# Optimization experiments

Measured on AMD Instinct MI355X. Metric: run time of the kernel, lower is better.

## Reference

```python
import jax, jax.numpy as jnp
import numpy as np

N_NODES = 500_000
N_EDGES = 5_000_000


def _glorot(key, shape):
    fan_in, fan_out = shape[0], shape[1]
    s = jnp.sqrt(6.0 / (fan_in + fan_out))
    return jax.random.uniform(key, shape, jnp.float32, -s, s)


def setup_inputs() -> dict:
    key = jax.random.key(0)
    ks = jax.random.split(key, 16)
    x = jax.random.normal(ks[0], (N_NODES, 3), jnp.float32)
    edge_index = jax.random.randint(ks[1], (2, N_EDGES), 0, N_NODES, jnp.int64)
    dims = [(3, 16), (16, 16), (16, 1)]
    inp = {"x": x, "edge_index": edge_index}
    for i, (din, dout) in enumerate(dims, start=1):
        k = jax.random.split(ks[1 + i], 5)
        inp[f"p{i}_w"] = _glorot(k[0], (din, din))   # project lin (bias=True)
        inp[f"p{i}_b"] = jnp.zeros((din,), jnp.float32)
        inp[f"l{i}_w"] = _glorot(k[1], (din, dout))  # lin_l on aggregated neighbors (bias=True)
        inp[f"l{i}_b"] = jnp.zeros((dout,), jnp.float32)
        inp[f"r{i}_w"] = _glorot(k[2], (din, dout))  # lin_r on root (bias=False)
    return inp


def _sage_conv(x, src, dst, pw, pb, lw, lb, rw):
    # project=True: neighbor messages use relu(lin(x)); root term uses original x
    h = jax.nn.relu(x @ pw + pb)                    # [N, din]
    msg = jnp.take(h, src, axis=0)                  # [E, din] gather from source j
    agg = jax.ops.segment_sum(msg, dst, num_segments=N_NODES)  # scatter-add to target i
    return agg @ lw + lb + x @ rw                   # [N, dout]


def reference(x, edge_index, p1_w, p1_b, l1_w, l1_b, r1_w,
              p2_w, p2_b, l2_w, l2_b, r2_w,
              p3_w, p3_b, l3_w, l3_b, r3_w):
    src, dst = edge_index[0], edge_index[1]
    h = jax.nn.relu(_sage_conv(x, src, dst, p1_w, p1_b, l1_w, l1_b, r1_w))
    h = jax.nn.relu(_sage_conv(h, src, dst, p2_w, p2_b, l2_w, l2_b, r2_w))
    return jax.nn.sigmoid(_sage_conv(h, src, dst, p3_w, p3_b, l3_w, l3_b, r3_w))
```

## Files before the change

### kernel.cpp

```cpp
#include <hip/hip_runtime.h>
#include <hip/hip_fp16.h>
#include <math.h>

#define NN 500000
#define NE 5000000
#define K_B 977
#define NBP 500
#define EPB 10000
#define CAP 6144
#define SEG 3072
#define PH 16
#define PHW 32768

__device__ inline float2 cvt2(unsigned u) {
    __half2 h = *reinterpret_cast<const __half2*>(&u);
    return __half22float2(h);
}

__device__ inline int wave_iscan(int x, int lane) {
#pragma unroll
    for (int d = 1; d < 64; d <<= 1) {
        int u = __shfl_up(x, d);
        if (lane >= d) x += u;
    }
    return x;
}


__global__ __launch_bounds__(512) void part_kernel(
    const int* __restrict__ ei, int* __restrict__ counts,
    unsigned int* __restrict__ edg_staged,
    const float* __restrict__ x, const float* __restrict__ p1w,
    const float* __restrict__ p1b, __half* __restrict__ h1)
{
    __shared__ unsigned stage[EPB];
    __shared__ int hist[1024];
    __shared__ int wsum[8];
    int t = threadIdx.x, j = blockIdx.x;
    int e0 = j * EPB;
    hist[t] = 0; hist[t + 512] = 0;
    __syncthreads();
    for (int k = t; k < EPB; k += 512) {
        int d = ei[NE + e0 + k];
        atomicAdd(&hist[d >> 9], 1);
    }
    __syncthreads();
    int v0 = hist[2*t], v1 = hist[2*t+1];
    int sv2 = v0 + v1;
    int lane = t & 63, w = t >> 6;
    int inc = wave_iscan(sv2, lane);
    if (lane == 63) wsum[w] = inc;
    __syncthreads();
    if (t == 0) {
        int run = 0;
#pragma unroll
        for (int i = 0; i < 8; ++i) { int tm = wsum[i]; wsum[i] = run; run += tm; }
    }
    __syncthreads();
    int excl = inc - sv2 + wsum[w];
    hist[2*t] = excl;
    hist[2*t+1] = excl + v0;
    if (2*t < K_B)   counts[j*K_B + 2*t]   = excl;
    if (2*t+1 < K_B) counts[j*K_B + 2*t+1] = excl + v0;
    __syncthreads();
    for (int k = t; k < EPB; k += 512) {
        int e = e0 + k;
        int sv = ei[e];
        int d = ei[NE + e];
        int pos = atomicAdd(&hist[d >> 9], 1);
        stage[pos] = ((unsigned)(d & 511) << 20) | (unsigned)sv;
    }
    __syncthreads();
    for (int k = t; k < EPB; k += 512)
        edg_staged[e0 + k] = stage[k];
    for (int i = j * 1000 + t; i < j * 1000 + 1000; i += 512) {
        float x0 = x[i*3+0], x1 = x[i*3+1], x2v = x[i*3+2];
        __half hh[4];
#pragma unroll
        for (int jj = 0; jj < 3; ++jj) {
            float v = fmaf(x0, p1w[0*3+jj], fmaf(x1, p1w[1*3+jj], fmaf(x2v, p1w[2*3+jj], p1b[jj])));
            hh[jj] = __float2half(v > 0.f ? v : 0.f);
        }
        hh[3] = __float2half(0.f);
        *reinterpret_cast<uint2*>(h1 + (size_t)i * 4) = *reinterpret_cast<uint2*>(hh);
    }
}


__global__ __launch_bounds__(512) void csrfin_l1(
    const int* __restrict__ counts,
    const unsigned int* __restrict__ edg_staged,
    const __half* __restrict__ h1, const float* __restrict__ x,
    const float* __restrict__ l1w, const float* __restrict__ l1b,
    const float* __restrict__ r1w,
    const float* __restrict__ p2w, const float* __restrict__ p2b,
    unsigned int* __restrict__ edg_fin, unsigned int* __restrict__ rowptr,
    __half* __restrict__ X2, __half* __restrict__ H2)
{
    __shared__ unsigned ebuf[CAP];
    __shared__ unsigned ebuf2[CAP];
    __shared__ unsigned cnt[4096];
    __shared__ int wsum[8];
    __shared__ int sh_total;
    __shared__ float slw[48], srw[48], slb[16], sp2w[256], sp2b[16];
    int b = blockIdx.x, t = threadIdx.x;
    if (t < 256) sp2w[t] = p2w[t];
    if (t < 48) { slw[t] = l1w[t]; srw[t] = r1w[t]; }
    if (t < 16) { slb[t] = l1b[t]; sp2b[t] = p2b[t]; }
    int pj = 0, lj = 0;
    if (t < NBP) {
        int base = t * K_B;
        int w0 = counts[base + b];
        int nx = (b == K_B - 1) ? EPB : counts[base + b + 1];
        pj = t * EPB + w0;
        lj = nx - w0;
    }
    int lane = t & 63, w = t >> 6;
    int inc = wave_iscan(lj, lane);
    if (lane == 63) wsum[w] = inc;
    __syncthreads();
    if (t == 0) {
        int run = 0;
#pragma unroll
        for (int i = 0; i < 8; ++i) { int tm = wsum[i]; wsum[i] = run; run += tm; }
        sh_total = run;
    }
    cnt[t] = 0; cnt[t + 512] = 0; cnt[t + 1024] = 0; cnt[t + 1536] = 0;
    cnt[t + 2048] = 0; cnt[t + 2560] = 0; cnt[t + 3072] = 0; cnt[t + 3584] = 0;
    __syncthreads();
    int poff = inc - lj + wsum[w];
    {
        int k = 0;
        for (; k + 4 <= lj; k += 4) {
            unsigned a0 = edg_staged[pj + k + 0];
            unsigned a1 = edg_staged[pj + k + 1];
            unsigned a2 = edg_staged[pj + k + 2];
            unsigned a3 = edg_staged[pj + k + 3];
            int p = poff + k;
            if (p + 3 < CAP) {
                ebuf[p + 0] = a0; ebuf[p + 1] = a1;
                ebuf[p + 2] = a2; ebuf[p + 3] = a3;
            } else {
                if (p + 0 < CAP) ebuf[p + 0] = a0;
                if (p + 1 < CAP) ebuf[p + 1] = a1;
                if (p + 2 < CAP) ebuf[p + 2] = a2;
                if (p + 3 < CAP) ebuf[p + 3] = a3;
            }
        }
        for (; k < lj; ++k) {
            int p = poff + k;
            if (p < CAP) ebuf[p] = edg_staged[pj + k];
        }
    }
    __syncthreads();
    int n2 = sh_total; if (n2 > CAP) n2 = CAP;
    for (int k = t; k < n2; k += 512) {
        unsigned v = ebuf[k];
        unsigned bin = ((v >> 20) << 4) | ((v & 0xFFFFFu) >> 15);
        atomicAdd(&cnt[bin >> 1], (bin & 1u) ? 65536u : 1u);
    }
    __syncthreads();
    unsigned wlo[8];
#pragma unroll
    for (int q = 0; q < 8; ++q) wlo[q] = cnt[t * 8 + q];
    int myc = 0;
#pragma unroll
    for (int q = 0; q < 8; ++q) myc += (int)(wlo[q] & 0xFFFFu) + (int)(wlo[q] >> 16);
    int inc2 = wave_iscan(myc, lane);
    if (lane == 63) wsum[w] = inc2;
    __syncthreads();
    if (t == 0) {
        int run = 0;
#pragma unroll
        for (int i = 0; i < 8; ++i) { int tm = wsum[i]; wsum[i] = run; run += tm; }
    }
    __syncthreads();
    int excl = inc2 - myc + wsum[w];
    int node = (b << 9) + t;
    unsigned gbase = (unsigned)(b * CAP + excl);
    if (node < NN) rowptr[node] = (gbase << 9) | (unsigned)myc;
    {
        int run2 = excl;
#pragma unroll
        for (int q = 0; q < 8; ++q) {
            int c0 = (int)(wlo[q] & 0xFFFFu), c1 = (int)(wlo[q] >> 16);
            cnt[t * 8 + q] = (unsigned)run2 | ((unsigned)(run2 + c0) << 16);
            run2 += c0 + c1;
        }
    }
    __syncthreads();
    for (int k = t; k < n2; k += 512) {
        unsigned v = ebuf[k];
        unsigned src = v & 0xFFFFFu;
        unsigned bin = ((v >> 20) << 4) | (src >> 15);
        unsigned old = atomicAdd(&cnt[bin >> 1], (bin & 1u) ? 65536u : 1u);
        unsigned pos = (bin & 1u) ? (old >> 16) : (old & 0xFFFFu);
        ebuf2[pos] = src;
    }
    __syncthreads();
    int bbase = b * CAP;
    for (int k = t; k < n2; k += 512) edg_fin[bbase + k] = ebuf2[k];
    if (node >= NN) return;
    float a0 = 0.f, a1 = 0.f, a2 = 0.f;
    for (int k = 0; k < myc; ++k) {
        unsigned s = ebuf2[excl + k];
        uint2 r = *reinterpret_cast<const uint2*>(h1 + (size_t)s * 4);
        float2 p0 = cvt2(r.x), q0 = cvt2(r.y);
        a0 += p0.x; a1 += p0.y; a2 += q0.x;
    }
    float x0 = x[node*3+0], x1 = x[node*3+1], x2v = x[node*3+2];
    float h[16];
#pragma unroll
    for (int j = 0; j < 16; ++j) {
        float v = slb[j];
        v = fmaf(a0, slw[j], fmaf(a1, slw[16+j], fmaf(a2, slw[32+j], v)));
        v = fmaf(x0, srw[j], fmaf(x1, srw[16+j], fmaf(x2v, srw[32+j], v)));
        h[j] = v > 0.f ? v : 0.f;
    }
    __half hx[16];
#pragma unroll
    for (int j = 0; j < 16; ++j) hx[j] = __float2half(h[j]);
    uint4* xp = reinterpret_cast<uint4*>(X2 + (size_t)node * 16);
    xp[0] = reinterpret_cast<uint4*>(hx)[0];
    xp[1] = reinterpret_cast<uint4*>(hx)[1];
    __half hh[16];
#pragma unroll
    for (int j = 0; j < 16; ++j) {
        float v = sp2b[j];
#pragma unroll
        for (int k = 0; k < 16; ++k) v = fmaf(h[k], sp2w[k*16+j], v);
        hh[j] = __float2half(v > 0.f ? v : 0.f);
    }
    uint4* hp = reinterpret_cast<uint4*>(H2 + (size_t)node * 16);
    hp[0] = reinterpret_cast<uint4*>(hh)[0];
    hp[1] = reinterpret_cast<uint4*>(hh)[1];
}


__global__ __launch_bounds__(256, 8) void layer2_kernel(
    const unsigned int* __restrict__ rowptr, const unsigned int* __restrict__ edg,
    const __half* __restrict__ H2, __half* X ,
    const float* __restrict__ l2w, const float* __restrict__ l2b,
    const float* __restrict__ r2w,
    const float* __restrict__ p3w, const float* __restrict__ p3b,
    const float* __restrict__ l3w, __half* __restrict__ g)
{
    __shared__ float slw[256], srw[256], sp3w[256];
    __shared__ float slb[16], sp3b[16], sl3w[16];
    __shared__ unsigned sedg[SEG];
    __shared__ int sred[256];
    int t = threadIdx.x;
    slw[t] = l2w[t]; srw[t] = r2w[t]; sp3w[t] = p3w[t];
    if (t < 16) { slb[t] = l2b[t]; sp3b[t] = p3b[t]; sl3w[t] = l3w[t]; }
    int i = blockIdx.x * 256 + t;
    bool act = i < NN;
    unsigned rp = act ? rowptr[i] : 0;
    int beg = (int)(rp >> 9), deg = act ? (int)(rp & 511u) : 0;
    sred[t] = act ? (beg + deg) : 0;
    __syncthreads();
    int base = (int)(rowptr[blockIdx.x * 256] >> 9);
    for (int off = 128; off > 0; off >>= 1) {
        if (t < off) { int o = sred[t + off]; if (o > sred[t]) sred[t] = o; }
        __syncthreads();
    }
    int seglen = sred[0] - base;
    if (seglen > SEG) seglen = SEG;
    for (int k = t; k < seglen; k += 256) sedg[k] = edg[base + k];
    __syncthreads();
    int e = beg - base, eend = e + deg;
    if (eend > SEG) eend = SEG;
    float av[16];
#pragma unroll
    for (int k = 0; k < 16; ++k) av[k] = 0.f;
#pragma unroll 1
    for (int p = 1; p <= PH; ++p) {
        unsigned lim = (unsigned)(p * PHW);
        while (e < eend) {
            unsigned s0 = sedg[e];
            if (s0 >= lim) break;
            const uint4* r0 = reinterpret_cast<const uint4*>(H2 + (size_t)s0 * 16);
            uint4 A0 = r0[0], B0 = r0[1];
            float2 f;
            f = cvt2(A0.x); av[0] += f.x; av[1] += f.y;
            f = cvt2(A0.y); av[2] += f.x; av[3] += f.y;
            f = cvt2(A0.z); av[4] += f.x; av[5] += f.y;
            f = cvt2(A0.w); av[6] += f.x; av[7] += f.y;
            f = cvt2(B0.x); av[8] += f.x; av[9] += f.y;
            f = cvt2(B0.y); av[10] += f.x; av[11] += f.y;
            f = cvt2(B0.z); av[12] += f.x; av[13] += f.y;
            f = cvt2(B0.w); av[14] += f.x; av[15] += f.y;
            ++e;
        }
        __syncthreads();
    }
    if (!act) return;
    float xv[16];
    const uint4* xp = reinterpret_cast<const uint4*>(X + (size_t)i * 16);
    uint4 XA = xp[0], XB = xp[1];
    {
        float2 f;
        f = cvt2(XA.x); xv[0] = f.x; xv[1] = f.y;
        f = cvt2(XA.y); xv[2] = f.x; xv[3] = f.y;
        f = cvt2(XA.z); xv[4] = f.x; xv[5] = f.y;
        f = cvt2(XA.w); xv[6] = f.x; xv[7] = f.y;
        f = cvt2(XB.x); xv[8] = f.x; xv[9] = f.y;
        f = cvt2(XB.y); xv[10] = f.x; xv[11] = f.y;
        f = cvt2(XB.z); xv[12] = f.x; xv[13] = f.y;
        f = cvt2(XB.w); xv[14] = f.x; xv[15] = f.y;
    }
    float o[16];
#pragma unroll
    for (int j = 0; j < 16; ++j) {
        float v = slb[j];
#pragma unroll
        for (int k = 0; k < 16; ++k) v = fmaf(av[k], slw[k*16+j], v);
#pragma unroll
        for (int k = 0; k < 16; ++k) v = fmaf(xv[k], srw[k*16+j], v);
        o[j] = v > 0.f ? v : 0.f;
    }
    __half ho[16];
#pragma unroll
    for (int j = 0; j < 16; ++j) ho[j] = __float2half(o[j]);
    uint4* op = reinterpret_cast<uint4*>(X + (size_t)i * 16);
    op[0] = reinterpret_cast<uint4*>(ho)[0];
    op[1] = reinterpret_cast<uint4*>(ho)[1];
    float gg = 0.f;
#pragma unroll
    for (int j = 0; j < 16; ++j) {
        float u = sp3b[j];
#pragma unroll
        for (int k = 0; k < 16; ++k) u = fmaf(o[k], sp3w[k*16+j], u);
        u = u > 0.f ? u : 0.f;
        gg = fmaf(u, sl3w[j], gg);
    }
    g[i] = __float2half(gg);
}


__global__ __launch_bounds__(256) void layer3_kernel(
    const unsigned int* __restrict__ rowptr, const unsigned int* __restrict__ edg,
    const __half* __restrict__ g, const __half* __restrict__ X,
    const float* __restrict__ l3b, const float* __restrict__ r3w,
    float* __restrict__ out)
{
    __shared__ float srw[16];
    __shared__ float sb;
    int t = threadIdx.x;
    if (t < 16) srw[t] = r3w[t];
    if (t == 0) sb = l3b[0];
    __syncthreads();
    int i = blockIdx.x * 256 + t;
    if (i >= NN) return;
    unsigned rp = rowptr[i];
    int beg = (int)(rp >> 9), deg = (int)(rp & 511u);
    int end = beg + deg;
    float a = 0.f;
    int e = beg;
    for (; e + 1 < end; e += 2) {
        int s0 = (int)edg[e], s1 = (int)edg[e+1];
        __half g0 = g[s0], g1 = g[s1];
        a += __half2float(g0) + __half2float(g1);
    }
    if (e < end) a += __half2float(g[(int)edg[e]]);
    float val = a + sb;
    const uint4* xp = reinterpret_cast<const uint4*>(X + (size_t)i * 16);
    uint4 XA = xp[0], XB = xp[1];
    float2 f;
    f = cvt2(XA.x); val = fmaf(f.x, srw[0], fmaf(f.y, srw[1], val));
    f = cvt2(XA.y); val = fmaf(f.x, srw[2], fmaf(f.y, srw[3], val));
    f = cvt2(XA.z); val = fmaf(f.x, srw[4], fmaf(f.y, srw[5], val));
    f = cvt2(XA.w); val = fmaf(f.x, srw[6], fmaf(f.y, srw[7], val));
    f = cvt2(XB.x); val = fmaf(f.x, srw[8], fmaf(f.y, srw[9], val));
    f = cvt2(XB.y); val = fmaf(f.x, srw[10], fmaf(f.y, srw[11], val));
    f = cvt2(XB.z); val = fmaf(f.x, srw[12], fmaf(f.y, srw[13], val));
    f = cvt2(XB.w); val = fmaf(f.x, srw[14], fmaf(f.y, srw[15], val));
    out[i] = 1.f / (1.f + expf(-val));
}


extern "C" void kernel_launch(void* const* d_in, const int* in_sizes, int n_in,
                              void* d_out, int out_size, void* d_ws, size_t ws_size,
                              hipStream_t stream) {
    const float* x   = (const float*)d_in[0];
    const int*   ei  = (const int*)d_in[1];
    const float* p1w = (const float*)d_in[2];
    const float* p1b = (const float*)d_in[3];
    const float* l1w = (const float*)d_in[4];
    const float* l1b = (const float*)d_in[5];
    const float* r1w = (const float*)d_in[6];
    const float* p2w = (const float*)d_in[7];
    const float* p2b = (const float*)d_in[8];
    const float* l2w = (const float*)d_in[9];
    const float* l2b = (const float*)d_in[10];
    const float* r2w = (const float*)d_in[11];
    const float* p3w = (const float*)d_in[12];
    const float* p3b = (const float*)d_in[13];
    const float* l3w = (const float*)d_in[14];
    const float* l3b = (const float*)d_in[15];
    const float* r3w = (const float*)d_in[16];
    float* out = (float*)d_out;

    char* ws = (char*)d_ws;
    __half*       X        = (__half*)(ws);
    __half*       H2       = (__half*)(ws + 16000000);
    unsigned int* edg_stg  = (unsigned int*)(ws + 32000000);
    unsigned int* edg_fin  = (unsigned int*)(ws + 52000000);
    __half*       h1       = (__half*)(ws + 76012288);
    __half*       g        = (__half*)(ws + 80012288);
    unsigned int* rowptr   = (unsigned int*)(ws + 81012288);
    int*          counts   = (int*)(ws + 83012288);

    const int nbN = (NN + 255) / 256;

    part_kernel<<<NBP, 512, 0, stream>>>(ei, counts, edg_stg, x, p1w, p1b, h1);
    csrfin_l1<<<K_B, 512, 0, stream>>>(counts, edg_stg, h1, x,
                                       l1w, l1b, r1w, p2w, p2b,
                                       edg_fin, rowptr, X, H2);
    layer2_kernel<<<nbN, 256, 0, stream>>>(rowptr, edg_fin, H2, X,
                                           l2w, l2b, r2w, p3w, p3b, l3w, g);
    layer3_kernel<<<nbN, 256, 0, stream>>>(rowptr, edg_fin, g, X, l3b, r3w, out);
}
```

Before: 178.8 us.

## Aggregate layer-1 neighbor features edge-parallel with LDS atomics

Layer-1 aggregation used to loop serially per destination node over its edges, which leaves threads idle when degrees are uneven. It now runs edge-parallel across the block: each thread handles two edges per step, gathers the fp16 source features, and adds them into a shared-memory per-destination accumulator with atomics. The sorted edge buffer now keeps the full packed value so the destination is available, and a barrier is added before nodes read their sums. This trades serial per-node loops for LDS float atomic contention and one extra sync, and the summation order is no longer deterministic.

```diff
diff --git a/kernel.cpp b/kernel.cpp
--- a/kernel.cpp
+++ b/kernel.cpp
@@ -100,6 +100,7 @@
     __shared__ unsigned ebuf[CAP];
     __shared__ unsigned ebuf2[CAP];
     __shared__ unsigned cnt[4096];
+    __shared__ float acc[3 * 512];
     __shared__ int wsum[8];
     __shared__ int sh_total;
     __shared__ float slw[48], srw[48], slb[16], sp2w[256], sp2b[16];
@@ -107,6 +108,7 @@
     if (t < 256) sp2w[t] = p2w[t];
     if (t < 48) { slw[t] = l1w[t]; srw[t] = r1w[t]; }
     if (t < 16) { slb[t] = l1b[t]; sp2b[t] = p2b[t]; }
+    acc[t] = 0.f; acc[t + 512] = 0.f; acc[t + 1024] = 0.f;
     int pj = 0, lj = 0;
     if (t < NBP) {
         int base = t * K_B;
@@ -191,23 +193,47 @@
     __syncthreads();
     for (int k = t; k < n2; k += 512) {
         unsigned v = ebuf[k];
-        unsigned src = v & 0xFFFFFu;
-        unsigned bin = ((v >> 20) << 4) | (src >> 15);
+        unsigned bin = ((v >> 20) << 4) | ((v & 0xFFFFFu) >> 15);
         unsigned old = atomicAdd(&cnt[bin >> 1], (bin & 1u) ? 65536u : 1u);
         unsigned pos = (bin & 1u) ? (old >> 16) : (old & 0xFFFFu);
-        ebuf2[pos] = src;
+        ebuf2[pos] = v;
     }
     __syncthreads();
     int bbase = b * CAP;
-    for (int k = t; k < n2; k += 512) edg_fin[bbase + k] = ebuf2[k];
+    {
+        int k = t;
+        for (; k + 512 < n2; k += 1024) {
+            unsigned v0 = ebuf2[k], v1 = ebuf2[k + 512];
+            unsigned s0 = v0 & 0xFFFFFu, s1 = v1 & 0xFFFFFu;
+            edg_fin[bbase + k] = s0;
+            edg_fin[bbase + k + 512] = s1;
+            int d0 = (int)(v0 >> 20), d1 = (int)(v1 >> 20);
+            uint2 r0 = *reinterpret_cast<const uint2*>(h1 + (size_t)s0 * 4);
+            uint2 r1 = *reinterpret_cast<const uint2*>(h1 + (size_t)s1 * 4);
+            float2 p0 = cvt2(r0.x), q0 = cvt2(r0.y);
+            atomicAdd(&acc[d0], p0.x);
+            atomicAdd(&acc[512 + d0], p0.y);
+            atomicAdd(&acc[1024 + d0], q0.x);
+            float2 p1 = cvt2(r1.x), q1 = cvt2(r1.y);
+            atomicAdd(&acc[d1], p1.x);
+            atomicAdd(&acc[512 + d1], p1.y);
+            atomicAdd(&acc[1024 + d1], q1.x);
+        }
+        if (k < n2) {
+            unsigned v0 = ebuf2[k];
+            unsigned s0 = v0 & 0xFFFFFu;
+            edg_fin[bbase + k] = s0;
+            int d0 = (int)(v0 >> 20);
+            uint2 r0 = *reinterpret_cast<const uint2*>(h1 + (size_t)s0 * 4);
+            float2 p0 = cvt2(r0.x), q0 = cvt2(r0.y);
+            atomicAdd(&acc[d0], p0.x);
+            atomicAdd(&acc[512 + d0], p0.y);
+            atomicAdd(&acc[1024 + d0], q0.x);
+        }
+    }
+    __syncthreads();
     if (node >= NN) return;
-    float a0 = 0.f, a1 = 0.f, a2 = 0.f;
-    for (int k = 0; k < myc; ++k) {
-        unsigned s = ebuf2[excl + k];
-        uint2 r = *reinterpret_cast<const uint2*>(h1 + (size_t)s * 4);
-        float2 p0 = cvt2(r.x), q0 = cvt2(r.y);
-        a0 += p0.x; a1 += p0.y; a2 += q0.x;
-    }
+    float a0 = acc[t], a1 = acc[512 + t], a2 = acc[1024 + t];
     float x0 = x[node*3+0], x1 = x[node*3+1], x2v = x[node*3+2];
     float h[16];
 #pragma unroll
```

After: 255.4 us. 42.8% more time.

## Process two rows per thread in layer2 and align blocks to CSR partitions

Applied to the files above, without the earlier changes.

The layer-2 kernel now has each 256-thread block cover 512 nodes, one CSR partition of CAP edges. Each thread aggregates two rows with interleaved gather loops. The block loads its edge segment straight from the known partition base, which drops the max-reduction over row ends and the SEG truncation. The source-index phase loop goes from 16 phases of 32768 to 8 phases of 65536, so there are fewer barriers. Occupancy is lowered to 5 blocks per CU and register pressure rises from the doubled accumulators, in exchange for more memory-level parallelism per thread.

```diff
diff --git a/kernel.cpp b/kernel.cpp
--- a/kernel.cpp
+++ b/kernel.cpp
@@ -8,9 +8,7 @@
 #define NBP 500
 #define EPB 10000
 #define CAP 6144
-#define SEG 3072
-#define PH 16
-#define PHW 32768
+#define PH 8
 
 __device__ inline float2 cvt2(unsigned u) {
     __half2 h = *reinterpret_cast<const __half2*>(&u);
@@ -237,63 +235,12 @@
 }
 
 
-__global__ __launch_bounds__(256, 8) void layer2_kernel(
-    const unsigned int* __restrict__ rowptr, const unsigned int* __restrict__ edg,
-    const __half* __restrict__ H2, __half* X ,
-    const float* __restrict__ l2w, const float* __restrict__ l2b,
-    const float* __restrict__ r2w,
-    const float* __restrict__ p3w, const float* __restrict__ p3b,
-    const float* __restrict__ l3w, __half* __restrict__ g)
+__device__ inline void l2_row(int i, const float* av,
+                              const float* slw, const float* srw,
+                              const float* slb, const float* sp3w,
+                              const float* sp3b, const float* sl3w,
+                              __half* X, __half* g)
 {
-    __shared__ float slw[256], srw[256], sp3w[256];
-    __shared__ float slb[16], sp3b[16], sl3w[16];
-    __shared__ unsigned sedg[SEG];
-    __shared__ int sred[256];
-    int t = threadIdx.x;
-    slw[t] = l2w[t]; srw[t] = r2w[t]; sp3w[t] = p3w[t];
-    if (t < 16) { slb[t] = l2b[t]; sp3b[t] = p3b[t]; sl3w[t] = l3w[t]; }
-    int i = blockIdx.x * 256 + t;
-    bool act = i < NN;
-    unsigned rp = act ? rowptr[i] : 0;
-    int beg = (int)(rp >> 9), deg = act ? (int)(rp & 511u) : 0;
-    sred[t] = act ? (beg + deg) : 0;
-    __syncthreads();
-    int base = (int)(rowptr[blockIdx.x * 256] >> 9);
-    for (int off = 128; off > 0; off >>= 1) {
-        if (t < off) { int o = sred[t + off]; if (o > sred[t]) sred[t] = o; }
-        __syncthreads();
-    }
-    int seglen = sred[0] - base;
-    if (seglen > SEG) seglen = SEG;
-    for (int k = t; k < seglen; k += 256) sedg[k] = edg[base + k];
-    __syncthreads();
-    int e = beg - base, eend = e + deg;
-    if (eend > SEG) eend = SEG;
-    float av[16];
-#pragma unroll
-    for (int k = 0; k < 16; ++k) av[k] = 0.f;
-#pragma unroll 1
-    for (int p = 1; p <= PH; ++p) {
-        unsigned lim = (unsigned)(p * PHW);
-        while (e < eend) {
-            unsigned s0 = sedg[e];
-            if (s0 >= lim) break;
-            const uint4* r0 = reinterpret_cast<const uint4*>(H2 + (size_t)s0 * 16);
-            uint4 A0 = r0[0], B0 = r0[1];
-            float2 f;
-            f = cvt2(A0.x); av[0] += f.x; av[1] += f.y;
-            f = cvt2(A0.y); av[2] += f.x; av[3] += f.y;
-            f = cvt2(A0.z); av[4] += f.x; av[5] += f.y;
-            f = cvt2(A0.w); av[6] += f.x; av[7] += f.y;
-            f = cvt2(B0.x); av[8] += f.x; av[9] += f.y;
-            f = cvt2(B0.y); av[10] += f.x; av[11] += f.y;
-            f = cvt2(B0.z); av[12] += f.x; av[13] += f.y;
-            f = cvt2(B0.w); av[14] += f.x; av[15] += f.y;
-            ++e;
-        }
-        __syncthreads();
-    }
-    if (!act) return;
     float xv[16];
     const uint4* xp = reinterpret_cast<const uint4*>(X + (size_t)i * 16);
     uint4 XA = xp[0], XB = xp[1];
@@ -334,6 +281,78 @@
         gg = fmaf(u, sl3w[j], gg);
     }
     g[i] = __float2half(gg);
+}
+
+__global__ __launch_bounds__(256, 5) void layer2_kernel(
+    const unsigned int* __restrict__ rowptr, const unsigned int* __restrict__ edg,
+    const __half* __restrict__ H2, __half* X ,
+    const float* __restrict__ l2w, const float* __restrict__ l2b,
+    const float* __restrict__ r2w,
+    const float* __restrict__ p3w, const float* __restrict__ p3b,
+    const float* __restrict__ l3w, __half* __restrict__ g)
+{
+    __shared__ float slw[256], srw[256], sp3w[256];
+    __shared__ float slb[16], sp3b[16], sl3w[16];
+    __shared__ unsigned sedg[CAP];
+    int t = threadIdx.x, b = blockIdx.x;
+    slw[t] = l2w[t]; srw[t] = r2w[t]; sp3w[t] = p3w[t];
+    if (t < 16) { slb[t] = l2b[t]; sp3b[t] = p3b[t]; sl3w[t] = l3w[t]; }
+    int base = b * CAP;
+    int iA = b * 512 + t;
+    int iB = iA + 256;
+    bool actB = iB < NN;
+    unsigned rpA = rowptr[iA];
+    unsigned rpB = actB ? rowptr[iB] : 0;
+    int eA = (int)(rpA >> 9) - base, dgA = (int)(rpA & 511u);
+    int eB = actB ? ((int)(rpB >> 9) - base) : 0, dgB = actB ? (int)(rpB & 511u) : 0;
+    int endA = eA + dgA, endB = eB + dgB;
+    int lastn = (b * 512 + 511 < NN) ? (b * 512 + 511) : (NN - 1);
+    unsigned rpl = rowptr[lastn];
+    int n2 = (int)(rpl >> 9) + (int)(rpl & 511u) - base;
+    for (int k = t; k < n2; k += 256) sedg[k] = edg[base + k];
+    __syncthreads();
+    float avA[16], avB[16];
+#pragma unroll
+    for (int k = 0; k < 16; ++k) { avA[k] = 0.f; avB[k] = 0.f; }
+#pragma unroll 1
+    for (int p = 1; p <= PH; ++p) {
+        unsigned lim = (unsigned)(p << 16);
+        while (eA < endA) {
+            unsigned s0 = sedg[eA];
+            if (s0 >= lim) break;
+            const uint4* r0 = reinterpret_cast<const uint4*>(H2 + (size_t)s0 * 16);
+            uint4 A0 = r0[0], B0 = r0[1];
+            float2 f;
+            f = cvt2(A0.x); avA[0] += f.x; avA[1] += f.y;
+            f = cvt2(A0.y); avA[2] += f.x; avA[3] += f.y;
+            f = cvt2(A0.z); avA[4] += f.x; avA[5] += f.y;
+            f = cvt2(A0.w); avA[6] += f.x; avA[7] += f.y;
+            f = cvt2(B0.x); avA[8] += f.x; avA[9] += f.y;
+            f = cvt2(B0.y); avA[10] += f.x; avA[11] += f.y;
+            f = cvt2(B0.z); avA[12] += f.x; avA[13] += f.y;
+            f = cvt2(B0.w); avA[14] += f.x; avA[15] += f.y;
+            ++eA;
+        }
+        while (eB < endB) {
+            unsigned s0 = sedg[eB];
+            if (s0 >= lim) break;
+            const uint4* r0 = reinterpret_cast<const uint4*>(H2 + (size_t)s0 * 16);
+            uint4 A0 = r0[0], B0 = r0[1];
+            float2 f;
+            f = cvt2(A0.x); avB[0] += f.x; avB[1] += f.y;
+            f = cvt2(A0.y); avB[2] += f.x; avB[3] += f.y;
+            f = cvt2(A0.z); avB[4] += f.x; avB[5] += f.y;
+            f = cvt2(A0.w); avB[6] += f.x; avB[7] += f.y;
+            f = cvt2(B0.x); avB[8] += f.x; avB[9] += f.y;
+            f = cvt2(B0.y); avB[10] += f.x; avB[11] += f.y;
+            f = cvt2(B0.z); avB[12] += f.x; avB[13] += f.y;
+            f = cvt2(B0.w); avB[14] += f.x; avB[15] += f.y;
+            ++eB;
+        }
+        __syncthreads();
+    }
+    l2_row(iA, avA, slw, srw, slb, sp3w, sp3b, sl3w, X, g);
+    if (actB) l2_row(iB, avB, slw, srw, slb, sp3w, sp3b, sl3w, X, g);
 }
 
 
@@ -416,7 +435,7 @@
     csrfin_l1<<<K_B, 512, 0, stream>>>(counts, edg_stg, h1, x,
                                        l1w, l1b, r1w, p2w, p2b,
                                        edg_fin, rowptr, X, H2);
-    layer2_kernel<<<nbN, 256, 0, stream>>>(rowptr, edg_fin, H2, X,
+    layer2_kernel<<<K_B, 256, 0, stream>>>(rowptr, edg_fin, H2, X,
                                            l2w, l2b, r2w, p3w, p3b, l3w, g);
     layer3_kernel<<<nbN, 256, 0, stream>>>(rowptr, edg_fin, g, X, l3b, r3w, out);
 }
```

Result: slower. 479.8 us (+168.3%).
